# Performance work log

Hardware: AMD Instinct MI355X
Metric: run time of the kernel (lower is better)

Reference implementation:

```python
import jax, jax.numpy as jnp
import numpy as np

EPS = 1e-5
NUM_GROUPS = 32
NUM_HEADS = 4


def setup_inputs() -> dict:
    key = jax.random.key(0)
    k1, k2, k3 = jax.random.split(key, 3)
    b, c, h, w = 8, 256, 32, 32
    x = jax.random.normal(k1, (b, c, h, w), dtype=jnp.float32)
    gn_w = jnp.ones((c,), dtype=jnp.float32)
    gn_b = jnp.zeros((c,), dtype=jnp.float32)
    qkv_w = jax.random.normal(k2, (3 * c, c), dtype=jnp.float32) * (1.0 / np.sqrt(c))
    qkv_b = jnp.zeros((3 * c,), dtype=jnp.float32)
    proj_w = jax.random.normal(k3, (c, c), dtype=jnp.float32) * (1.0 / np.sqrt(c))
    proj_b = jnp.zeros((c,), dtype=jnp.float32)
    return {"x": x, "gn_w": gn_w, "gn_b": gn_b, "qkv_w": qkv_w,
            "qkv_b": qkv_b, "proj_w": proj_w, "proj_b": proj_b}


def _group_norm(x, weight, bias):
    # x: (b, c, n)
    b, c, n = x.shape
    xg = x.reshape(b, NUM_GROUPS, (c // NUM_GROUPS) * n)
    mean = jnp.mean(xg, axis=-1, keepdims=True)
    var = jnp.mean(jnp.square(xg - mean), axis=-1, keepdims=True)
    xn = ((xg - mean) * jax.lax.rsqrt(var + EPS)).reshape(b, c, n)
    return xn * weight[None, :, None] + bias[None, :, None]


def reference(x, gn_w, gn_b, qkv_w, qkv_b, proj_w, proj_b):
    b, c, h, w = x.shape
    # FFT2 over spatial dims, then view_as_real -> flatten: seq len N = 2*h*w
    xf = jnp.fft.fft2(x)                                   # (b,c,h,w) complex64
    xr = jnp.stack([xf.real, xf.imag], axis=-1).reshape(b, c, -1)  # (b,c,N)
    n = xr.shape[-1]
    # GroupNorm(32, c) then 1x1 Conv1d producing qkv
    normed = _group_norm(xr, gn_w, gn_b)
    qkv = jnp.einsum('oc,bcn->bon', qkv_w, normed) + qkv_b[None, :, None]  # (b,3c,N)
    # split heads exactly like torch: view(b*H, 3c/H, N) then split along dim 1
    qkv = qkv.reshape(b * NUM_HEADS, 3 * c // NUM_HEADS, n)
    ch = c // NUM_HEADS
    q, k, v = qkv[:, :ch], qkv[:, ch:2 * ch], qkv[:, 2 * ch:]
    scale = ch ** -0.25
    weight = jnp.einsum('bct,bcs->bts', q * scale, k * scale)  # (b*H, N, N)
    weight = jax.nn.softmax(weight, axis=-1)
    a = jnp.einsum('bts,bcs->bct', weight, v).reshape(b, c, n)
    out = jnp.einsum('oc,bcn->bon', proj_w, a) + proj_b[None, :, None]  # (b,c,N)
    # back to complex and IFFT2
    out = out.reshape(b, c, h, w, 2)
    oc = jax.lax.complex(out[..., 0], out[..., 1])
    res = jnp.fft.ifft2(oc)                                # (b,c,h,w) complex64
    # return complex result as real/imag pair
    return jnp.stack([res.real, res.imag], axis=-1)         # (b,c,h,w,2)
```

## Files before the change

kernel.cpp:

```cpp
#include <hip/hip_runtime.h>
#include <hip/hip_bf16.h>
#include <stdint.h>

#define PI_F 3.14159265358979323846f
#define C1_EXP 0.18033688f
#define C2_EXP 23.083120f

typedef __bf16 bf16x8 __attribute__((ext_vector_type(8)));
typedef float f32x4 __attribute__((ext_vector_type(4)));
typedef unsigned int uint32x4 __attribute__((ext_vector_type(4)));

#define BAR_LDS() asm volatile("s_waitcnt lgkmcnt(0)\n\ts_barrier" ::: "memory")

__device__ __forceinline__ bf16x8 neg8(bf16x8 v) {
  union { bf16x8 b; uint32x4 u; } x;
  x.b = v;
  x.u ^= (uint32x4){0x80008000u, 0x80008000u, 0x80008000u, 0x80008000u};
  return x.b;
}

#define MFMA3(acc, Ph, Pl, Qh, Ql)                                        \
  acc = __builtin_amdgcn_mfma_f32_16x16x32_bf16(Ph, Qh, acc, 0, 0, 0);    \
  acc = __builtin_amdgcn_mfma_f32_16x16x32_bf16(Ph, Ql, acc, 0, 0, 0);    \
  acc = __builtin_amdgcn_mfma_f32_16x16x32_bf16(Pl, Qh, acc, 0, 0, 0);

__device__ __forceinline__ int slot2n(int slot) {
  const int pi = slot >> 1, im = slot & 1;
  int k1, k2;
  if (pi < 480)      { k1 = 1 + (pi >> 5); k2 = pi & 31; }
  else if (pi < 495) { k1 = 0;  k2 = pi - 479; }
  else if (pi < 510) { k1 = 16; k2 = pi - 494; }
  else if (pi < 514) { k1 = ((pi - 510) >> 1) * 16; k2 = ((pi - 510) & 1) * 16; }
  else               { k1 = 0; k2 = 0; }
  return 2 * (k1 * 32 + k2) + im;
}

__global__ __launch_bounds__(256) void k_twid(__bf16* __restrict__ tw) {
  for (int e = threadIdx.x; e < 1024; e += 256) {
    const int j = e >> 5, k = e & 31;
    const int t = (j * k) & 31;
    float sv, cv;
    sincosf(2.0f * PI_F * (float)t / 32.0f, &sv, &cv);
    const __bf16 ch = (__bf16)cv;
    const __bf16 sh = (__bf16)sv;
    tw[e] = ch;
    tw[1024 + e] = (__bf16)(cv - (float)ch);
    tw[2048 + e] = sh;
    tw[3072 + e] = (__bf16)(sv - (float)sh);
  }
}

__global__ __launch_bounds__(256) void k_fft2(const float* __restrict__ x,
                                              float* __restrict__ xr,
                                              float* __restrict__ stats_raw,
                                              const __bf16* __restrict__ tw) {
  __shared__ __align__(16) char smem[51200];
  const int tid = threadIdx.x, lane = tid & 63, wv = tid >> 6;
  const int quad = lane >> 4, q16 = lane & 15;
  const int slice = blockIdx.x * 4 + wv;
  char* const wr_ = smem + 10240 + wv * 10240;

  const float* xs = x + (size_t)slice * 1024;
  float4 xv[4];
#pragma unroll
  for (int u = 0; u < 4; ++u) xv[u] = ((const float4*)xs)[u * 64 + lane];

  for (int i = tid; i < 512; i += 256) {
    const int t = i >> 7, r = (i >> 2) & 31, c8 = (i & 3) * 8;
    *(uint4*)(smem + t * 2560 + r * 80 + c8 * 2) =
        *(const uint4*)(tw + t * 1024 + r * 32 + c8);
  }

#pragma unroll
  for (int u = 0; u < 4; ++u) {
    const int f = u * 64 + lane;
    const float4 v = xv[u];
    const int row = f >> 3, c4 = (f & 7) * 4;
    union { unsigned long long q; __bf16 b[4]; } ph, pl;
    ph.b[0] = (__bf16)v.x; ph.b[1] = (__bf16)v.y;
    ph.b[2] = (__bf16)v.z; ph.b[3] = (__bf16)v.w;
    pl.b[0] = (__bf16)(v.x - (float)ph.b[0]);
    pl.b[1] = (__bf16)(v.y - (float)ph.b[1]);
    pl.b[2] = (__bf16)(v.z - (float)ph.b[2]);
    pl.b[3] = (__bf16)(v.w - (float)ph.b[3]);
    *(unsigned long long*)(wr_ + row * 80 + c4 * 2) = ph.q;
    *(unsigned long long*)(wr_ + 2560 + row * 80 + c4 * 2) = pl.q;
  }
  __syncthreads();

  bf16x8 cch[2], ccl[2], ssh[2], ssl[2], xh[2], xl[2];
#pragma unroll
  for (int t2 = 0; t2 < 2; ++t2) {
    const int row = t2 * 16 + q16;
    cch[t2] = *(const bf16x8*)(smem + row * 80 + quad * 16);
    ccl[t2] = *(const bf16x8*)(smem + 2560 + row * 80 + quad * 16);
    ssh[t2] = *(const bf16x8*)(smem + 5120 + row * 80 + quad * 16);
    ssl[t2] = *(const bf16x8*)(smem + 7680 + row * 80 + quad * 16);
    xh[t2] = *(const bf16x8*)(wr_ + row * 80 + quad * 16);
    xl[t2] = *(const bf16x8*)(wr_ + 2560 + row * 80 + quad * 16);
  }

  f32x4 yre[2][2] = {}, yim[2][2] = {};
#pragma unroll
  for (int mt = 0; mt < 2; ++mt)
#pragma unroll
    for (int nt = 0; nt < 2; ++nt) {
      MFMA3(yre[mt][nt], xh[mt], xl[mt], cch[nt], ccl[nt]);
      MFMA3(yim[mt][nt], xh[mt], xl[mt], ssh[nt], ssl[nt]);
    }

#pragma unroll
  for (int mt = 0; mt < 2; ++mt)
#pragma unroll
    for (int nt = 0; nt < 2; ++nt) {
      char* base = wr_ + (nt * 16 + q16) * 80 + (mt * 16 + quad * 4) * 2;
      union { unsigned long long q; __bf16 b[4]; } h, l;
#pragma unroll
      for (int r = 0; r < 4; ++r) {
        const float v = yre[mt][nt][r];
        h.b[r] = (__bf16)v; l.b[r] = (__bf16)(v - (float)h.b[r]);
      }
      *(unsigned long long*)(base) = h.q;
      *(unsigned long long*)(base + 2560) = l.q;
#pragma unroll
      for (int r = 0; r < 4; ++r) {
        const float v = -yim[mt][nt][r];
        h.b[r] = (__bf16)v; l.b[r] = (__bf16)(v - (float)h.b[r]);
      }
      *(unsigned long long*)(base + 5120) = h.q;
      *(unsigned long long*)(base + 7680) = l.q;
    }
  asm volatile("" ::: "memory");

  bf16x8 yreh[2], yrel[2], yimh[2], yiml[2];
#pragma unroll
  for (int nt = 0; nt < 2; ++nt) {
    const int row = nt * 16 + q16;
    yreh[nt] = *(const bf16x8*)(wr_ + row * 80 + quad * 16);
    yrel[nt] = *(const bf16x8*)(wr_ + 2560 + row * 80 + quad * 16);
    yimh[nt] = *(const bf16x8*)(wr_ + 5120 + row * 80 + quad * 16);
    yiml[nt] = *(const bf16x8*)(wr_ + 7680 + row * 80 + quad * 16);
  }

  f32x4 zre[2][2] = {}, zim[2][2] = {};
  bf16x8 ssnh[2], ssnl[2];
  ssnh[0] = neg8(ssh[0]); ssnh[1] = neg8(ssh[1]);
  ssnl[0] = neg8(ssl[0]); ssnl[1] = neg8(ssl[1]);
#pragma unroll
  for (int mt = 0; mt < 2; ++mt)
#pragma unroll
    for (int nt = 0; nt < 2; ++nt) {
      MFMA3(zre[mt][nt], cch[mt], ccl[mt], yreh[nt], yrel[nt]);
      MFMA3(zre[mt][nt], ssh[mt], ssl[mt], yimh[nt], yiml[nt]);
      MFMA3(zim[mt][nt], cch[mt], ccl[mt], yimh[nt], yiml[nt]);
      MFMA3(zim[mt][nt], ssnh[mt], ssnl[mt], yreh[nt], yrel[nt]);
    }

  float* op = xr + (size_t)slice * 2048;
  float s1 = 0.f, s2 = 0.f;
#pragma unroll
  for (int mt = 0; mt < 2; ++mt)
#pragma unroll
    for (int nt = 0; nt < 2; ++nt)
#pragma unroll
      for (int r = 0; r < 4; ++r) {
        const int k1 = mt * 16 + quad * 4 + r;
        const int k2 = nt * 16 + q16;
        const float a = zre[mt][nt][r], bimg = zim[mt][nt][r];
        s1 += a + bimg;
        s2 += a * a + bimg * bimg;
        float2 st; st.x = a; st.y = bimg;
        *(float2*)(op + 2 * (k1 * 32 + k2)) = st;
      }
#pragma unroll
  for (int off = 1; off <= 32; off <<= 1) {
    s1 += __shfl_xor(s1, off);
    s2 += __shfl_xor(s2, off);
  }
  if (lane == 0) {
    const int bg = (slice >> 8) * 32 + ((slice & 255) >> 3);
    atomicAdd(&stats_raw[bg * 2], s1);
    atomicAdd(&stats_raw[bg * 2 + 1], s2);
  }
}

__global__ __launch_bounds__(256) void k_uvec(const float* __restrict__ stats_raw,
                                              const float* __restrict__ gn_w,
                                              const float* __restrict__ gn_b,
                                              const float* __restrict__ qkv_w,
                                              const float* __restrict__ qkv_b,
                                              float* __restrict__ uk,
                                              float* __restrict__ uv) {
  const int blk = blockIdx.x;
  const int tid = threadIdx.x;
  const int b = blk >> 3, h = (blk >> 1) & 3, role = blk & 1;
  __shared__ float Bsh[256];
  {
    const int g = tid >> 3;
    const float S = stats_raw[(b * 32 + g) * 2];
    const float S2 = stats_raw[(b * 32 + g) * 2 + 1];
    const float mean = S * (1.0f / 16384.0f);
    const float var = S2 * (1.0f / 16384.0f) - mean * mean;
    const float rstd = rsqrtf(var + 1e-5f);
    Bsh[tid] = gn_b[tid] - mean * rstd * gn_w[tid];
  }
  __syncthreads();
  const int cp = tid >> 2, seg = tid & 3;
  const int row = h * 192 + 64 + role * 64 + cp;
  const float* wr_ = qkv_w + (size_t)row * 256 + seg * 64;
  const float* bs = Bsh + seg * 64;
  float s = 0.f;
#pragma unroll
  for (int i = 0; i < 16; ++i) {
    const float4 w4 = *(const float4*)(wr_ + i * 4);
    const float4 b4 = *(const float4*)(bs + i * 4);
    s += w4.x * b4.x + w4.y * b4.y + w4.z * b4.z + w4.w * b4.w;
  }
  s += __shfl_xor(s, 1);
  s += __shfl_xor(s, 2);
  if (seg == 0) {
    float* dst = (role == 0) ? uk : uv;
    dst[(size_t)(b * 4 + h) * 64 + cp] = s + qkv_b[row];
  }
}

__global__ __launch_bounds__(256) void k_gntrans(const float* __restrict__ xr,
                                                 const float* __restrict__ stats_raw,
                                                 const float* __restrict__ w,
                                                 const float* __restrict__ bias,
                                                 __bf16* __restrict__ xt) {
  const int n0 = blockIdx.x * 64;
  const int c0 = blockIdx.y * 64;
  const int b = blockIdx.z;
  __shared__ __bf16 Lt[64][72];
  const int tid = threadIdx.x;
  for (int i = tid; i < 1024; i += 256) {
    const int cl = i >> 4, c = c0 + cl, nl = (i & 15) * 4;
    const float S = stats_raw[(b * 32 + (c >> 3)) * 2];
    const float S2 = stats_raw[(b * 32 + (c >> 3)) * 2 + 1];
    const float mean = S * (1.0f / 16384.0f);
    const float var = S2 * (1.0f / 16384.0f) - mean * mean;
    const float rstd = rsqrtf(var + 1e-5f);
    const float sc = rstd * w[c];
    const float sh = bias[c] - mean * sc;
    const float4 v = *(const float4*)(xr + ((size_t)b * 256 + c) * 2048 + n0 + nl);
    Lt[nl][cl] = (__bf16)(v.x * sc + sh);
    Lt[nl + 1][cl] = (__bf16)(v.y * sc + sh);
    Lt[nl + 2][cl] = (__bf16)(v.z * sc + sh);
    Lt[nl + 3][cl] = (__bf16)(v.w * sc + sh);
  }
  __syncthreads();
  __bf16* dst = xt + (size_t)b * 524288 + (size_t)n0 * 256 + c0;
  for (int i = tid; i < 512; i += 256) {
    const int nl = i >> 3, cch = (i & 7) * 8;
    *(uint4*)(dst + (size_t)nl * 256 + cch) = *(const uint4*)&Lt[nl][cch];
  }
}

__global__ __launch_bounds__(256) void k_gemm_qkv(const float* __restrict__ W,
                                                  const __bf16* __restrict__ X,
                                                  const float* __restrict__ bias,
                                                  const float* __restrict__ uk,
                                                  float* __restrict__ dq,
                                                  __bf16* __restrict__ Qt,
                                                  __bf16* __restrict__ Kt,
                                                  __bf16* __restrict__ Vt) {
  const int tx = blockIdx.x;
  const int b = blockIdx.y;
  int role, hd, nt;
  if (tx < 64) { role = 0; hd = tx >> 4; nt = tx & 15; }
  else if (tx < 100) { role = 1; const int i = tx - 64; hd = i / 9; nt = i - hd * 9; }
  else { role = 2; const int i = tx - 100; hd = i / 9; nt = i - hd * 9; }
  const int n0 = nt * 128;
  const int bo = hd * 192 + role * 64;
  const __bf16* Xb = X + (size_t)b * 524288;

  __shared__ __align__(16) char smem[30720];
  __bf16 (*Ot)[72] = (__bf16(*)[72])smem;
  __bf16 (*Ot2)[136] = (__bf16(*)[136])smem;

  const int tid = threadIdx.x, lane = tid & 63, wv = tid >> 6;
  const int quad = lane >> 4, q16 = lane & 15, wn = wv * 32;

  const int rowA = tid >> 2, chA = (tid & 3) * 8;
  const int browB0 = tid >> 2, bchB = (tid & 3) * 8;
  const float* wA = W + (size_t)(bo + rowA) * 256 + chA;

  const int s0r = n0 + browB0, s1r = n0 + browB0 + 64;
  const int pn0 = (role == 0) ? s0r : slot2n(s0r);
  const int pn1 = (role == 0) ? s1r : slot2n(s1r);

  float4 aP0 = *(const float4*)(wA);
  float4 aP1 = *(const float4*)(wA + 4);
  uint4 bP0 = *(const uint4*)(Xb + (size_t)pn0 * 256 + bchB);
  uint4 bP1 = *(const uint4*)(Xb + (size_t)pn1 * 256 + bchB);

  f32x4 acc[4][2] = {};
  int bsel = 0;
  for (int k0 = 0; k0 < 256; k0 += 32) {
    char* const Ab = smem + bsel;
    char* const Bb = smem + bsel + 5120;
    {
      union { uint4 u; __bf16 h[8]; } pa;
      pa.h[0] = (__bf16)aP0.x; pa.h[1] = (__bf16)aP0.y;
      pa.h[2] = (__bf16)aP0.z; pa.h[3] = (__bf16)aP0.w;
      pa.h[4] = (__bf16)aP1.x; pa.h[5] = (__bf16)aP1.y;
      pa.h[6] = (__bf16)aP1.z; pa.h[7] = (__bf16)aP1.w;
      *(uint4*)(Ab + rowA * 80 + chA * 2) = pa.u;
      *(uint4*)(Bb + browB0 * 80 + bchB * 2) = bP0;
      *(uint4*)(Bb + (browB0 + 64) * 80 + bchB * 2) = bP1;
    }
    __syncthreads();
    if (k0 + 32 < 256) {
      const int kn = k0 + 32;
      aP0 = *(const float4*)(wA + kn);
      aP1 = *(const float4*)(wA + kn + 4);
      bP0 = *(const uint4*)(Xb + (size_t)pn0 * 256 + kn + bchB);
      bP1 = *(const uint4*)(Xb + (size_t)pn1 * 256 + kn + bchB);
    }
    bf16x8 af[4], bfr[2];
#pragma unroll
    for (int mt = 0; mt < 4; ++mt)
      af[mt] = *(const bf16x8*)(Ab + (mt * 16 + q16) * 80 + quad * 16);
#pragma unroll
    for (int jn = 0; jn < 2; ++jn)
      bfr[jn] = *(const bf16x8*)(Bb + (wn + jn * 16 + q16) * 80 + quad * 16);
#pragma unroll
    for (int mt = 0; mt < 4; ++mt)
#pragma unroll
      for (int jn = 0; jn < 2; ++jn)
        acc[mt][jn] = __builtin_amdgcn_mfma_f32_16x16x32_bf16(af[mt], bfr[jn], acc[mt][jn], 0, 0, 0);
    bsel ^= 15360;
  }
  __syncthreads();

  const int bh = b * 4 + hd;
  if (role == 2) {
#pragma unroll
    for (int mt = 0; mt < 4; ++mt)
#pragma unroll
      for (int r = 0; r < 4; ++r) {
        const int c = mt * 16 + quad * 4 + r;
        const float bv = bias[bo + c];
#pragma unroll
        for (int jn = 0; jn < 2; ++jn)
          Ot2[c][wn + jn * 16 + q16] = (__bf16)(acc[mt][jn][r] + bv);
      }
    __syncthreads();
    __bf16* dst = Vt + (size_t)bh * 73728;
    for (int i = tid; i < 1024; i += 256) {
      const int c = i >> 4, sg = (i & 15) * 8;
      *(uint4*)(dst + (size_t)c * 1152 + n0 + sg) = *(const uint4*)&Ot2[c][sg];
    }
  } else {
    __bf16* dst = (role == 0 ? Qt + (size_t)bh * 131072
                             : Kt + (size_t)bh * 73728);
#pragma unroll
    for (int mt = 0; mt < 4; ++mt)
#pragma unroll
      for (int r = 0; r < 4; ++r) {
        const int c = mt * 16 + quad * 4 + r;
        const float bv = bias[bo + c];
#pragma unroll
        for (int jn = 0; jn < 2; ++jn)
          Ot[wn + jn * 16 + q16][c] = (__bf16)(acc[mt][jn][r] + bv);
      }
    __syncthreads();
    for (int i = tid; i < 1024; i += 256) {
      const int nl = i >> 3, cch = (i & 7) * 8;
      *(uint4*)(dst + (size_t)(n0 + nl) * 64 + cch) = *(const uint4*)&Ot[nl][cch];
    }
    if (role == 0 && tid < 128) {
      const float* ukp = uk + (size_t)bh * 64;
      float dv = 0.f;
#pragma unroll
      for (int g8 = 0; g8 < 8; ++g8) {
        const bf16x8 qv = *(const bf16x8*)&Ot[tid][g8 * 8];
#pragma unroll
        for (int k = 0; k < 8; ++k) dv += (float)qv[k] * ukp[g8 * 8 + k];
      }
      dq[(size_t)bh * 2048 + n0 + tid] = dv * (2.0f * C1_EXP);
    }
  }
}

template <bool EDGE>
__device__ __forceinline__ void attn_iter(
    const int s0, const int send, const int quad,
    const __bf16* __restrict__ kg, const __bf16* __restrict__ vg,
    char* const kw, char* const vw,
    const char* const (&krp)[2][2], const char* const (&vrp)[4],
    char* const (&pwp)[2][2], const char* const (&prp)[2],
    const bf16x8 (&bq)[2][2], const float (&Dm)[2],
    uint4& kA, uint4& vA, f32x4 (&oacc)[2][4],
    float (&lsum)[2], float (&spsum)[2]) {
  *(uint4*)kw = kA;
  *(uint4*)vw = vA;
  BAR_LDS();
  if (s0 + 32 < send) {
    kA = *(const uint4*)(kg + (size_t)(s0 + 32) * 64);
    vA = *(const uint4*)(vg + s0 + 32);
  }

  f32x4 sacc[2][2] = {};
#pragma unroll
  for (int j = 0; j < 2; ++j)
#pragma unroll
    for (int kk = 0; kk < 2; ++kk) {
      const bf16x8 ak = *(const bf16x8*)krp[j][kk];
      sacc[0][j] = __builtin_amdgcn_mfma_f32_16x16x32_bf16(ak, bq[0][kk], sacc[0][j], 0, 0, 0);
      sacc[1][j] = __builtin_amdgcn_mfma_f32_16x16x32_bf16(ak, bq[1][kk], sacc[1][j], 0, 0, 0);
    }

#pragma unroll
  for (int b = 0; b < 2; ++b) {
    float lacc = 0.f, spacc = 0.f;
#pragma unroll
    for (int j = 0; j < 2; ++j) {
      float B0, B2, Bv1, Bv3, Bm1, Bm3;
      if (EDGE) {
        const int sg = s0 + j * 16 + quad * 4;
        B0 = (sg < 1020) ? (1.0f - C2_EXP) : ((sg < 1028) ? -C2_EXP : -1e30f);
        B2 = (sg + 2 < 1020) ? (1.0f - C2_EXP)
                             : ((sg + 2 < 1028) ? -C2_EXP : -1e30f);
        Bv1 = (sg + 1 < 1028) ? -C2_EXP : -1e30f;
        Bv3 = (sg + 3 < 1028) ? -C2_EXP : -1e30f;
        Bm1 = (sg + 1 < 1020) ? Dm[b] : -1e30f;
        Bm3 = (sg + 3 < 1020) ? Dm[b] : -1e30f;
      } else {
        B0 = 1.0f - C2_EXP;
        B2 = 1.0f - C2_EXP;
        Bv1 = -C2_EXP;
        Bv3 = -C2_EXP;
        Bm1 = Dm[b];
        Bm3 = Dm[b];
      }
      const float P0  = __builtin_amdgcn_exp2f(fmaf(sacc[b][j][0],  C1_EXP, B0));
      const float Pv1 = __builtin_amdgcn_exp2f(fmaf(sacc[b][j][1],  C1_EXP, Bv1));
      const float P2  = __builtin_amdgcn_exp2f(fmaf(sacc[b][j][2],  C1_EXP, B2));
      const float Pv3 = __builtin_amdgcn_exp2f(fmaf(sacc[b][j][3],  C1_EXP, Bv3));
      const float pm1 = __builtin_amdgcn_exp2f(fmaf(sacc[b][j][1], -C1_EXP, Bm1));
      const float pm3 = __builtin_amdgcn_exp2f(fmaf(sacc[b][j][3], -C1_EXP, Bm3));
      const float mm = pm1 + pm3;
      lacc += (P0 + P2) + (Pv1 + Pv3) + mm;
      spacc += mm;
      union { uint2 u; __bf16 h[4]; } pk;
      pk.h[0] = (__bf16)P0;
      pk.h[1] = (__bf16)(Pv1 - pm1);
      pk.h[2] = (__bf16)P2;
      pk.h[3] = (__bf16)(Pv3 - pm3);
      *(uint2*)pwp[b][j] = pk.u;
    }
    lsum[b] += lacc;
    spsum[b] += spacc;
  }
  asm volatile("" ::: "memory");

  bf16x8 bp[2];
  bp[0] = *(const bf16x8*)prp[0];
  bp[1] = *(const bf16x8*)prp[1];
#pragma unroll
  for (int jc = 0; jc < 4; ++jc) {
    const bf16x8 av = *(const bf16x8*)vrp[jc];
    oacc[0][jc] = __builtin_amdgcn_mfma_f32_16x16x32_bf16(av, bp[0], oacc[0][jc], 0, 0, 0);
    oacc[1][jc] = __builtin_amdgcn_mfma_f32_16x16x32_bf16(av, bp[1], oacc[1][jc], 0, 0, 0);
  }
  BAR_LDS();
}

__global__ __launch_bounds__(256, 4) void k_attn_mfma(const __bf16* __restrict__ Qt,
                                                      const __bf16* __restrict__ Kt,
                                                      const __bf16* __restrict__ Vt,
                                                      const float* __restrict__ dq,
                                                      const float* __restrict__ uv,
                                                      __bf16* __restrict__ opart,
                                                      float* __restrict__ lpart) {
  const int t0 = blockIdx.x * 128;
  const int part = blockIdx.y;
  const int bh = blockIdx.z;
  const __bf16* kt = Kt + (size_t)bh * 73728;
  const __bf16* vt = Vt + (size_t)bh * 73728;

  __shared__ __align__(16) char smem[16384];

  const int tid = threadIdx.x, lane = tid & 63, wv = tid >> 6;
  const int quad = lane >> 4, q16 = lane & 15;
  const int wband = wv * 32;

  const int rK = tid >> 3, gK = tid & 7;
  char* const kw = smem + rK * 128 + ((gK ^ (rK & 7)) * 16);
  const int cV = tid >> 2, gV = tid & 3;
  char* const vw = smem + 4096 + (cV >> 1) * 128 +
                   ((((cV & 1) * 4 + gV) ^ ((cV >> 1) & 7)) * 16);
  const __bf16* const kg = kt + (size_t)rK * 64 + gK * 8;
  const __bf16* const vg = vt + (size_t)cV * 1152 + gV * 8;

  const char* krp[2][2];
#pragma unroll
  for (int j = 0; j < 2; ++j)
#pragma unroll
    for (int kk = 0; kk < 2; ++kk)
      krp[j][kk] = smem + (j * 16 + q16) * 128 + (((kk * 4 + quad) ^ (q16 & 7)) * 16);
  const int a7 = (q16 >> 1) & 7, p1 = q16 & 1;
  const char* vrp[4];
#pragma unroll
  for (int jc = 0; jc < 4; ++jc)
    vrp[jc] = smem + 4096 + (jc * 8 + (q16 >> 1)) * 128 +
              (((p1 * 4 + quad) ^ a7) * 16);
  char* pwp[2][2];
  const char* prp[2];
#pragma unroll
  for (int b = 0; b < 2; ++b) {
    const int mrow = ((wband + b * 16) >> 1) + (q16 >> 1);
    prp[b] = smem + 8192 + mrow * 128 + (((p1 * 4 + quad) ^ a7) * 16);
#pragma unroll
    for (int j = 0; j < 2; ++j)
      pwp[b][j] = smem + 8192 + mrow * 128 +
                  (((p1 * 4 + j * 2 + (quad >> 1)) ^ a7) * 16) + (quad & 1) * 8;
  }

  const __bf16* qbase = Qt + (size_t)bh * 131072;
  bf16x8 bq[2][2];
  float Dm[2];
#pragma unroll
  for (int b = 0; b < 2; ++b) {
    const int t = t0 + wband + b * 16 + q16;
    const __bf16* qp = qbase + (size_t)t * 64 + quad * 8;
    bq[b][0] = *(const bf16x8*)qp;
    bq[b][1] = *(const bf16x8*)(qp + 32);
    Dm[b] = dq[(size_t)bh * 2048 + t] - C2_EXP;
  }

  f32x4 oacc[2][4] = {};
  float lsum[2] = {0.f, 0.f};
  float spsum[2] = {0.f, 0.f};

  const int sbase = part * 352, send = sbase + 352;
  const int sInt = (part == 2) ? 992 : send;
  uint4 kA = *(const uint4*)(kg + (size_t)sbase * 64);
  uint4 vA = *(const uint4*)(vg + sbase);

  for (int s0 = sbase; s0 < sInt; s0 += 32)
    attn_iter<false>(s0, send, quad, kg, vg, kw, vw, krp, vrp, pwp, prp,
                     bq, Dm, kA, vA, oacc, lsum, spsum);
  for (int s0 = sInt; s0 < send; s0 += 32)
    attn_iter<true>(s0, send, quad, kg, vg, kw, vw, krp, vrp, pwp, prp,
                    bq, Dm, kA, vA, oacc, lsum, spsum);

  float4 uv4[4];
  {
    const float* uvp = uv + (size_t)bh * 64;
#pragma unroll
    for (int jc = 0; jc < 4; ++jc)
      uv4[jc] = *(const float4*)(uvp + jc * 16 + quad * 4);
  }

#pragma unroll
  for (int b = 0; b < 2; ++b) {
    float l = lsum[b], sp = spsum[b];
    l += __shfl_xor(l, 16);
    l += __shfl_xor(l, 32);
    sp += __shfl_xor(sp, 16);
    sp += __shfl_xor(sp, 32);
    const float sp2 = 2.0f * sp;
    const int t = t0 + wband + b * 16 + q16;
    const size_t row = (size_t)(bh * 3 + part) * 2048 + t;
    if (quad == 0) lpart[row] = l;
    __bf16* opp = opart + row * 64;
#pragma unroll
    for (int jc = 0; jc < 4; ++jc) {
      union { uint2 u; __bf16 h[4]; } pk;
      pk.h[0] = (__bf16)(oacc[b][jc][0] + sp2 * uv4[jc].x);
      pk.h[1] = (__bf16)(oacc[b][jc][1] + sp2 * uv4[jc].y);
      pk.h[2] = (__bf16)(oacc[b][jc][2] + sp2 * uv4[jc].z);
      pk.h[3] = (__bf16)(oacc[b][jc][3] + sp2 * uv4[jc].w);
      *(uint2*)(opp + jc * 16 + quad * 4) = pk.u;
    }
  }
}

__global__ __launch_bounds__(256) void k_gemm_proj(const float* __restrict__ W,
                                                   const __bf16* __restrict__ opart,
                                                   const float* __restrict__ lpart,
                                                   const float* __restrict__ bias,
                                                   float* __restrict__ C) {
  const int n0 = blockIdx.x * 128;
  const int bo = blockIdx.y * 64;
  const int b = blockIdx.z;
  float* Cb = C + (size_t)b * 524288;

  __shared__ __align__(16) char smem[30720];

  const int tid = threadIdx.x, lane = tid & 63, wv = tid >> 6;
  const int quad = lane >> 4, q16 = lane & 15, wn = wv * 32;

  const int rowA = tid >> 2, chA = (tid & 3) * 8;
  const int browB0 = tid >> 2, bchB = (tid & 3) * 8;
  const float* wA = W + (size_t)(bo + rowA) * 256 + chA;

  float linv[2][4];
#pragma unroll
  for (int g = 0; g < 2; ++g) {
    const int t = n0 + browB0 + g * 64;
#pragma unroll
    for (int hd = 0; hd < 4; ++hd) {
      const size_t rr = (size_t)((b * 4 + hd) * 3) * 2048 + t;
      linv[g][hd] = 1.0f / (lpart[rr] + lpart[rr + 2048] + lpart[rr + 4096]);
    }
  }

  float4 aP0 = *(const float4*)(wA);
  float4 aP1 = *(const float4*)(wA + 4);
  bf16x8 oP[2][3];
#pragma unroll
  for (int g = 0; g < 2; ++g) {
    const int t = n0 + browB0 + g * 64;
    const size_t rr = (size_t)(b * 4 * 3) * 2048 + t;
#pragma unroll
    for (int p = 0; p < 3; ++p)
      oP[g][p] = *(const bf16x8*)(opart + (rr + p * 2048) * 64 + bchB);
  }

  f32x4 acc[4][2] = {};
  int bsel = 0;
  for (int k0 = 0; k0 < 256; k0 += 32) {
    char* const Ab = smem + bsel;
    char* const Bb = smem + bsel + 5120;
    {
      union { uint4 u; __bf16 h[8]; } pa;
      pa.h[0] = (__bf16)aP0.x; pa.h[1] = (__bf16)aP0.y;
      pa.h[2] = (__bf16)aP0.z; pa.h[3] = (__bf16)aP0.w;
      pa.h[4] = (__bf16)aP1.x; pa.h[5] = (__bf16)aP1.y;
      pa.h[6] = (__bf16)aP1.z; pa.h[7] = (__bf16)aP1.w;
      *(uint4*)(Ab + rowA * 80 + chA * 2) = pa.u;
      const int hd = (k0 + bchB) >> 6;
#pragma unroll
      for (int g = 0; g < 2; ++g) {
        const float inv = linv[g][hd];
        bf16x8 res;
#pragma unroll
        for (int k = 0; k < 8; ++k)
          res[k] = (__bf16)((((float)oP[g][0][k] + (float)oP[g][1][k]) +
                             (float)oP[g][2][k]) * inv);
        *(bf16x8*)(Bb + (browB0 + g * 64) * 80 + bchB * 2) = res;
      }
    }
    __syncthreads();
    if (k0 + 32 < 256) {
      const int kn = k0 + 32;
      aP0 = *(const float4*)(wA + kn);
      aP1 = *(const float4*)(wA + kn + 4);
      const int c = kn + bchB;
      const int hd = c >> 6, cu = c & 63;
#pragma unroll
      for (int g = 0; g < 2; ++g) {
        const int t = n0 + browB0 + g * 64;
        const size_t rr = (size_t)((b * 4 + hd) * 3) * 2048 + t;
#pragma unroll
        for (int p = 0; p < 3; ++p)
          oP[g][p] = *(const bf16x8*)(opart + (rr + p * 2048) * 64 + cu);
      }
    }
    bf16x8 af[4], bfr[2];
#pragma unroll
    for (int mt = 0; mt < 4; ++mt)
      af[mt] = *(const bf16x8*)(Ab + (mt * 16 + q16) * 80 + quad * 16);
#pragma unroll
    for (int jn = 0; jn < 2; ++jn)
      bfr[jn] = *(const bf16x8*)(Bb + (wn + jn * 16 + q16) * 80 + quad * 16);
#pragma unroll
    for (int mt = 0; mt < 4; ++mt)
#pragma unroll
      for (int jn = 0; jn < 2; ++jn)
        acc[mt][jn] = __builtin_amdgcn_mfma_f32_16x16x32_bf16(af[mt], bfr[jn], acc[mt][jn], 0, 0, 0);
    bsel ^= 15360;
  }

#pragma unroll
  for (int mt = 0; mt < 4; ++mt)
#pragma unroll
    for (int r = 0; r < 4; ++r) {
      const int o = bo + mt * 16 + quad * 4 + r;
      const float bv = bias[o];
#pragma unroll
      for (int jn = 0; jn < 2; ++jn)
        Cb[(size_t)o * 2048 + n0 + wn + jn * 16 + q16] = acc[mt][jn][r] + bv;
    }
}

__global__ __launch_bounds__(256) void k_ifft2(const float* __restrict__ spec,
                                               float* __restrict__ out,
                                               const __bf16* __restrict__ tw) {
  __shared__ __align__(16) char smem[51200];
  const int tid = threadIdx.x, lane = tid & 63, wv = tid >> 6;
  const int quad = lane >> 4, q16 = lane & 15;
  const int slice = blockIdx.x * 4 + wv;
  char* const wr_ = smem + 10240 + wv * 10240;

  const float* sp = spec + (size_t)slice * 2048;
  float4 sv8[8];
#pragma unroll
  for (int u = 0; u < 8; ++u) sv8[u] = ((const float4*)sp)[u * 64 + lane];

  for (int i = tid; i < 512; i += 256) {
    const int t = i >> 7, r = (i >> 2) & 31, c8 = (i & 3) * 8;
    *(uint4*)(smem + t * 2560 + r * 80 + c8 * 2) =
        *(const uint4*)(tw + t * 1024 + r * 32 + c8);
  }

#pragma unroll
  for (int u = 0; u < 8; ++u) {
    const int f = u * 64 + lane;
    const float4 v = sv8[u];
    const int k1 = f >> 4, k2 = (f & 15) * 2;
    char* base = wr_ + k1 * 80 + k2 * 2;
    union { unsigned int w; __bf16 b[2]; } p;
    const __bf16 rh0 = (__bf16)v.x, rh1 = (__bf16)v.z;
    const __bf16 ih0 = (__bf16)v.y, ih1 = (__bf16)v.w;
    p.b[0] = rh0; p.b[1] = rh1; *(unsigned int*)(base) = p.w;
    p.b[0] = (__bf16)(v.x - (float)rh0);
    p.b[1] = (__bf16)(v.z - (float)rh1); *(unsigned int*)(base + 2560) = p.w;
    p.b[0] = ih0; p.b[1] = ih1; *(unsigned int*)(base + 5120) = p.w;
    p.b[0] = (__bf16)(v.y - (float)ih0);
    p.b[1] = (__bf16)(v.w - (float)ih1); *(unsigned int*)(base + 7680) = p.w;
  }
  __syncthreads();

  bf16x8 cch[2], ccl[2], ssh[2], ssl[2], ssnh[2], ssnl[2];
  bf16x8 xreh[2], xrel[2], ximh[2], ximl[2];
#pragma unroll
  for (int t2 = 0; t2 < 2; ++t2) {
    const int row = t2 * 16 + q16;
    cch[t2] = *(const bf16x8*)(smem + row * 80 + quad * 16);
    ccl[t2] = *(const bf16x8*)(smem + 2560 + row * 80 + quad * 16);
    ssh[t2] = *(const bf16x8*)(smem + 5120 + row * 80 + quad * 16);
    ssl[t2] = *(const bf16x8*)(smem + 7680 + row * 80 + quad * 16);
    xreh[t2] = *(const bf16x8*)(wr_ + row * 80 + quad * 16);
    xrel[t2] = *(const bf16x8*)(wr_ + 2560 + row * 80 + quad * 16);
    ximh[t2] = *(const bf16x8*)(wr_ + 5120 + row * 80 + quad * 16);
    ximl[t2] = *(const bf16x8*)(wr_ + 7680 + row * 80 + quad * 16);
  }
  ssnh[0] = neg8(ssh[0]); ssnh[1] = neg8(ssh[1]);
  ssnl[0] = neg8(ssl[0]); ssnl[1] = neg8(ssl[1]);

  f32x4 yre[2][2] = {}, yim[2][2] = {};
#pragma unroll
  for (int mt = 0; mt < 2; ++mt)
#pragma unroll
    for (int nt = 0; nt < 2; ++nt) {
      MFMA3(yre[mt][nt], xreh[mt], xrel[mt], cch[nt], ccl[nt]);
      MFMA3(yre[mt][nt], ximh[mt], ximl[mt], ssnh[nt], ssnl[nt]);
      MFMA3(yim[mt][nt], xreh[mt], xrel[mt], ssh[nt], ssl[nt]);
      MFMA3(yim[mt][nt], ximh[mt], ximl[mt], cch[nt], ccl[nt]);
    }

#pragma unroll
  for (int mt = 0; mt < 2; ++mt)
#pragma unroll
    for (int nt = 0; nt < 2; ++nt) {
      char* base = wr_ + (nt * 16 + q16) * 80 + (mt * 16 + quad * 4) * 2;
      union { unsigned long long q; __bf16 b[4]; } h, l;
#pragma unroll
      for (int r = 0; r < 4; ++r) {
        const float v = yre[mt][nt][r];
        h.b[r] = (__bf16)v; l.b[r] = (__bf16)(v - (float)h.b[r]);
      }
      *(unsigned long long*)(base) = h.q;
      *(unsigned long long*)(base + 2560) = l.q;
#pragma unroll
      for (int r = 0; r < 4; ++r) {
        const float v = yim[mt][nt][r];
        h.b[r] = (__bf16)v; l.b[r] = (__bf16)(v - (float)h.b[r]);
      }
      *(unsigned long long*)(base + 5120) = h.q;
      *(unsigned long long*)(base + 7680) = l.q;
    }
  asm volatile("" ::: "memory");

  bf16x8 yreh[2], yrel[2], yimh[2], yiml[2];
#pragma unroll
  for (int nt = 0; nt < 2; ++nt) {
    const int row = nt * 16 + q16;
    yreh[nt] = *(const bf16x8*)(wr_ + row * 80 + quad * 16);
    yrel[nt] = *(const bf16x8*)(wr_ + 2560 + row * 80 + quad * 16);
    yimh[nt] = *(const bf16x8*)(wr_ + 5120 + row * 80 + quad * 16);
    yiml[nt] = *(const bf16x8*)(wr_ + 7680 + row * 80 + quad * 16);
  }

  f32x4 zre[2][2] = {}, zim[2][2] = {};
#pragma unroll
  for (int mt = 0; mt < 2; ++mt)
#pragma unroll
    for (int nt = 0; nt < 2; ++nt) {
      MFMA3(zre[mt][nt], cch[mt], ccl[mt], yreh[nt], yrel[nt]);
      MFMA3(zre[mt][nt], ssnh[mt], ssnl[mt], yimh[nt], yiml[nt]);
      MFMA3(zim[mt][nt], cch[mt], ccl[mt], yimh[nt], yiml[nt]);
      MFMA3(zim[mt][nt], ssh[mt], ssl[mt], yreh[nt], yrel[nt]);
    }

  float* op = out + (size_t)slice * 2048;
#pragma unroll
  for (int mt = 0; mt < 2; ++mt)
#pragma unroll
    for (int nt = 0; nt < 2; ++nt)
#pragma unroll
      for (int r = 0; r < 4; ++r) {
        const int n1 = mt * 16 + quad * 4 + r;
        const int n2 = nt * 16 + q16;
        float2 st;
        st.x = zre[mt][nt][r] * (1.0f / 1024.0f);
        st.y = zim[mt][nt][r] * (1.0f / 1024.0f);
        *(float2*)(op + 2 * (n1 * 32 + n2)) = st;
      }
}

extern "C" void kernel_launch(void* const* d_in, const int* in_sizes, int n_in,
                              void* d_out, int out_size, void* d_ws, size_t ws_size,
                              hipStream_t stream) {
  (void)in_sizes; (void)n_in; (void)out_size; (void)ws_size;
  const float* x      = (const float*)d_in[0];
  const float* gn_w   = (const float*)d_in[1];
  const float* gn_b   = (const float*)d_in[2];
  const float* qkv_w  = (const float*)d_in[3];
  const float* qkv_b  = (const float*)d_in[4];
  const float* proj_w = (const float*)d_in[5];
  const float* proj_b = (const float*)d_in[6];
  float* out = (float*)d_out;

  float* spec  = (float*)d_ws;
  __bf16* Qt   = (__bf16*)(spec + 4194304);
  __bf16* Kt   = Qt + 4194304;
  __bf16* Vt   = Kt + 2359296;
  float* stats = (float*)(Vt + 2359296);
  float* xr    = stats + 512;
  __bf16* xt   = (__bf16*)(xr + 4194304);
  __bf16* opart = (__bf16*)xr;
  float*  lpart = (float*)(opart + 12582912);
  float*  dq    = lpart + 196608;
  float*  uk    = dq + 65536;
  float*  uv    = uk + 2048;
  __bf16* tw    = (__bf16*)(uv + 2048);

  hipMemsetAsync(stats, 0, 512 * sizeof(float), stream);
  k_twid<<<1, 256, 0, stream>>>(tw);
  k_fft2<<<512, 256, 0, stream>>>(x, xr, stats, tw);
  k_uvec<<<64, 256, 0, stream>>>(stats, gn_w, gn_b, qkv_w, qkv_b, uk, uv);
  k_gntrans<<<dim3(32, 4, 8), 256, 0, stream>>>(xr, stats, gn_w, gn_b, xt);
  k_gemm_qkv<<<dim3(136, 8), 256, 0, stream>>>(qkv_w, xt, qkv_b, uk, dq,
                                               Qt, Kt, Vt);
  k_attn_mfma<<<dim3(16, 3, 32), 256, 0, stream>>>(Qt, Kt, Vt, dq, uv,
                                                   opart, lpart);
  k_gemm_proj<<<dim3(16, 4, 8), 256, 0, stream>>>(proj_w, opart, lpart,
                                                  proj_b, spec);
  k_ifft2<<<512, 256, 0, stream>>>(spec, out, tw);
}
```

Before: 166.8 us.

## Drop split-KV partitioning in attention and normalize output in-kernel

The attention kernel no longer splits the key sequence into three partitions. Each block now processes the whole key range, normalizes its output by the row sum, and writes a single bf16 result. The projection GEMM then reads one partial instead of summing three and dividing by the summed lpart values. This removes the extra partial-output traffic and the reduction work in the projection, but the attention grid shrinks from 1536 to 512 blocks, which lowers parallelism and occupancy on the GPU.

```diff
diff --git a/kernel.cpp b/kernel.cpp
--- a/kernel.cpp
+++ b/kernel.cpp
@@ -473,11 +473,9 @@
                                                       const __bf16* __restrict__ Vt,
                                                       const float* __restrict__ dq,
                                                       const float* __restrict__ uv,
-                                                      __bf16* __restrict__ opart,
-                                                      float* __restrict__ lpart) {
+                                                      __bf16* __restrict__ opart) {
   const int t0 = blockIdx.x * 128;
-  const int part = blockIdx.y;
-  const int bh = blockIdx.z;
+  const int bh = blockIdx.y;
   const __bf16* kt = Kt + (size_t)bh * 73728;
   const __bf16* vt = Vt + (size_t)bh * 73728;
 
@@ -535,15 +533,14 @@
   float lsum[2] = {0.f, 0.f};
   float spsum[2] = {0.f, 0.f};
 
-  const int sbase = part * 352, send = sbase + 352;
-  const int sInt = (part == 2) ? 992 : send;
-  uint4 kA = *(const uint4*)(kg + (size_t)sbase * 64);
-  uint4 vA = *(const uint4*)(vg + sbase);
-
-  for (int s0 = sbase; s0 < sInt; s0 += 32)
+  const int send = 1056;
+  uint4 kA = *(const uint4*)(kg);
+  uint4 vA = *(const uint4*)(vg);
+
+  for (int s0 = 0; s0 < 992; s0 += 32)
     attn_iter<false>(s0, send, quad, kg, vg, kw, vw, krp, vrp, pwp, prp,
                      bq, Dm, kA, vA, oacc, lsum, spsum);
-  for (int s0 = sInt; s0 < send; s0 += 32)
+  for (int s0 = 992; s0 < send; s0 += 32)
     attn_iter<true>(s0, send, quad, kg, vg, kw, vw, krp, vrp, pwp, prp,
                     bq, Dm, kA, vA, oacc, lsum, spsum);
 
@@ -562,18 +559,17 @@
     l += __shfl_xor(l, 32);
     sp += __shfl_xor(sp, 16);
     sp += __shfl_xor(sp, 32);
-    const float sp2 = 2.0f * sp;
+    const float inv = 1.0f / l;
+    const float su = 2.0f * sp * inv;
     const int t = t0 + wband + b * 16 + q16;
-    const size_t row = (size_t)(bh * 3 + part) * 2048 + t;
-    if (quad == 0) lpart[row] = l;
-    __bf16* opp = opart + row * 64;
+    __bf16* opp = opart + ((size_t)bh * 2048 + t) * 64;
 #pragma unroll
     for (int jc = 0; jc < 4; ++jc) {
       union { uint2 u; __bf16 h[4]; } pk;
-      pk.h[0] = (__bf16)(oacc[b][jc][0] + sp2 * uv4[jc].x);
-      pk.h[1] = (__bf16)(oacc[b][jc][1] + sp2 * uv4[jc].y);
-      pk.h[2] = (__bf16)(oacc[b][jc][2] + sp2 * uv4[jc].z);
-      pk.h[3] = (__bf16)(oacc[b][jc][3] + sp2 * uv4[jc].w);
+      pk.h[0] = (__bf16)(oacc[b][jc][0] * inv + su * uv4[jc].x);
+      pk.h[1] = (__bf16)(oacc[b][jc][1] * inv + su * uv4[jc].y);
+      pk.h[2] = (__bf16)(oacc[b][jc][2] * inv + su * uv4[jc].z);
+      pk.h[3] = (__bf16)(oacc[b][jc][3] * inv + su * uv4[jc].w);
       *(uint2*)(opp + jc * 16 + quad * 4) = pk.u;
     }
   }
@@ -581,7 +577,6 @@
 
 __global__ __launch_bounds__(256) void k_gemm_proj(const float* __restrict__ W,
                                                    const __bf16* __restrict__ opart,
-                                                   const float* __restrict__ lpart,
                                                    const float* __restrict__ bias,
                                                    float* __restrict__ C) {
   const int n0 = blockIdx.x * 128;
@@ -598,27 +593,14 @@
   const int browB0 = tid >> 2, bchB = (tid & 3) * 8;
   const float* wA = W + (size_t)(bo + rowA) * 256 + chA;
 
-  float linv[2][4];
+  float4 aP0 = *(const float4*)(wA);
+  float4 aP1 = *(const float4*)(wA + 4);
+  uint4 oPd[2];
 #pragma unroll
   for (int g = 0; g < 2; ++g) {
     const int t = n0 + browB0 + g * 64;
-#pragma unroll
-    for (int hd = 0; hd < 4; ++hd) {
-      const size_t rr = (size_t)((b * 4 + hd) * 3) * 2048 + t;
-      linv[g][hd] = 1.0f / (lpart[rr] + lpart[rr + 2048] + lpart[rr + 4096]);
-    }
-  }
-
-  float4 aP0 = *(const float4*)(wA);
-  float4 aP1 = *(const float4*)(wA + 4);
-  bf16x8 oP[2][3];
-#pragma unroll
-  for (int g = 0; g < 2; ++g) {
-    const int t = n0 + browB0 + g * 64;
-    const size_t rr = (size_t)(b * 4 * 3) * 2048 + t;
-#pragma unroll
-    for (int p = 0; p < 3; ++p)
-      oP[g][p] = *(const bf16x8*)(opart + (rr + p * 2048) * 64 + bchB);
+    const size_t rr = (size_t)(b * 4) * 2048 + t;
+    oPd[g] = *(const uint4*)(opart + rr * 64 + bchB);
   }
 
   f32x4 acc[4][2] = {};
@@ -633,17 +615,8 @@
       pa.h[4] = (__bf16)aP1.x; pa.h[5] = (__bf16)aP1.y;
       pa.h[6] = (__bf16)aP1.z; pa.h[7] = (__bf16)aP1.w;
       *(uint4*)(Ab + rowA * 80 + chA * 2) = pa.u;
-      const int hd = (k0 + bchB) >> 6;
-#pragma unroll
-      for (int g = 0; g < 2; ++g) {
-        const float inv = linv[g][hd];
-        bf16x8 res;
-#pragma unroll
-        for (int k = 0; k < 8; ++k)
-          res[k] = (__bf16)((((float)oP[g][0][k] + (float)oP[g][1][k]) +
-                             (float)oP[g][2][k]) * inv);
-        *(bf16x8*)(Bb + (browB0 + g * 64) * 80 + bchB * 2) = res;
-      }
+      *(uint4*)(Bb + browB0 * 80 + bchB * 2) = oPd[0];
+      *(uint4*)(Bb + (browB0 + 64) * 80 + bchB * 2) = oPd[1];
     }
     __syncthreads();
     if (k0 + 32 < 256) {
@@ -655,10 +628,8 @@
 #pragma unroll
       for (int g = 0; g < 2; ++g) {
         const int t = n0 + browB0 + g * 64;
-        const size_t rr = (size_t)((b * 4 + hd) * 3) * 2048 + t;
-#pragma unroll
-        for (int p = 0; p < 3; ++p)
-          oP[g][p] = *(const bf16x8*)(opart + (rr + p * 2048) * 64 + cu);
+        const size_t rr = (size_t)(b * 4 + hd) * 2048 + t;
+        oPd[g] = *(const uint4*)(opart + rr * 64 + cu);
       }
     }
     bf16x8 af[4], bfr[2];
@@ -835,8 +806,7 @@
   float* xr    = stats + 512;
   __bf16* xt   = (__bf16*)(xr + 4194304);
   __bf16* opart = (__bf16*)xr;
-  float*  lpart = (float*)(opart + 12582912);
-  float*  dq    = lpart + 196608;
+  float*  dq    = (float*)(opart + 12582912);
   float*  uk    = dq + 65536;
   float*  uv    = uk + 2048;
   __bf16* tw    = (__bf16*)(uv + 2048);
@@ -848,9 +818,7 @@
   k_gntrans<<<dim3(32, 4, 8), 256, 0, stream>>>(xr, stats, gn_w, gn_b, xt);
   k_gemm_qkv<<<dim3(136, 8), 256, 0, stream>>>(qkv_w, xt, qkv_b, uk, dq,
                                                Qt, Kt, Vt);
-  k_attn_mfma<<<dim3(16, 3, 32), 256, 0, stream>>>(Qt, Kt, Vt, dq, uv,
-                                                   opart, lpart);
-  k_gemm_proj<<<dim3(16, 4, 8), 256, 0, stream>>>(proj_w, opart, lpart,
-                                                  proj_b, spec);
+  k_attn_mfma<<<dim3(16, 32), 256, 0, stream>>>(Qt, Kt, Vt, dq, uv, opart);
+  k_gemm_proj<<<dim3(16, 4, 8), 256, 0, stream>>>(proj_w, opart, proj_b, spec);
   k_ifft2<<<512, 256, 0, stream>>>(spec, out, tw);
 }
```

New measurement: 165.2 us. About the same (-1.0%).
